# Optimization experiments

Measured on AMD Instinct MI355X. Metric: run time of the kernel, lower is better.

## Reference

```python
import jax, jax.numpy as jnp
import numpy as np
import math

B, S, IN_DIM, FEATURES = 4, 4096, 1024, 1024


def setup_inputs() -> dict:
    key = jax.random.key(0)
    kx, kk = jax.random.split(key)
    x = jax.random.normal(kx, (B, S, IN_DIM), dtype=jnp.float32)
    # bool kernel representing a +1/-1 binary weight matrix
    kernel = jax.random.randint(kk, (IN_DIM, FEATURES), 0, 2).astype(jnp.bool_)
    scale = jnp.float32(1.0 / math.sqrt(IN_DIM))  # nn.initializers.constant(1/sqrt(in_dim))
    return {"x": x, "kernel": kernel, "scale": scale}


def reference(x, kernel, scale):
    # conn_dense: bool kernel encodes +1 (True) / -1 (False) weights
    w = jnp.where(kernel, 1.0, -1.0).astype(x.dtype)  # [in_dim, features]
    # [b, s, in] @ [in, f] -> [b, s, f], then scalar scale
    return scale * jnp.einsum("bsi,if->bsf", x, w)
```

## Files before the change

### kernel.cpp

```cpp
#include <hip/hip_runtime.h>


#define M_TOT 16384
#define N_TOT 1024
#define K_TOT 1024

typedef __attribute__((ext_vector_type(8))) short bf16x8;
typedef __attribute__((ext_vector_type(4))) float f32x4;

__device__ __forceinline__ unsigned short f2bf(float f) {
    unsigned int u = __builtin_bit_cast(unsigned int, f);
    u += 0x7FFFu + ((u >> 16) & 1u);
    return (unsigned short)(u >> 16);
}

__global__ void detect_mode(const unsigned int* __restrict__ k32, int* __restrict__ flag) {
    __shared__ int s;
    if (threadIdx.x == 0) s = 0;
    __syncthreads();
    int bad = 0;
    for (int i = threadIdx.x; i < 1024; i += 256)
        if (k32[i] > 1u) bad = 1;
    if (bad) atomicOr(&s, 1);
    __syncthreads();
    if (threadIdx.x == 0) flag[0] = s;
}

__global__ __launch_bounds__(256) void convert_w(
    const void* __restrict__ w_raw, unsigned short* __restrict__ wt,
    const int* __restrict__ mode_p)
{
    __shared__ unsigned short tile[64 * 72];
    const int tid = threadIdx.x;
    const int k0 = (blockIdx.x & 15) * 64;
    const int n0 = (blockIdx.x >> 4) * 64;
    const int row = tid >> 2;
    const int seg = (tid & 3) * 16;

    if (mode_p[0] == 0) {
        const unsigned int* w = (const unsigned int*)w_raw;
        const uint4* src = reinterpret_cast<const uint4*>(
            w + (size_t)(k0 + row) * N_TOT + n0 + seg);
        #pragma unroll
        for (int q = 0; q < 4; ++q) {
            uint4 v = src[q];
            ushort4 h;
            h.x = v.x ? 0x3F80u : 0xBF80u;
            h.y = v.y ? 0x3F80u : 0xBF80u;
            h.z = v.z ? 0x3F80u : 0xBF80u;
            h.w = v.w ? 0x3F80u : 0xBF80u;
            *reinterpret_cast<ushort4*>(&tile[row * 72 + seg + q * 4]) = h;
        }
    } else {
        const unsigned char* w = (const unsigned char*)w_raw;
        uint4 v = *reinterpret_cast<const uint4*>(
            w + (size_t)(k0 + row) * N_TOT + n0 + seg);
        unsigned char b[16];
        *reinterpret_cast<uint4*>(b) = v;
        #pragma unroll
        for (int q = 0; q < 4; ++q) {
            ushort4 h;
            h.x = b[q * 4 + 0] ? 0x3F80u : 0xBF80u;
            h.y = b[q * 4 + 1] ? 0x3F80u : 0xBF80u;
            h.z = b[q * 4 + 2] ? 0x3F80u : 0xBF80u;
            h.w = b[q * 4 + 3] ? 0x3F80u : 0xBF80u;
            *reinterpret_cast<ushort4*>(&tile[row * 72 + seg + q * 4]) = h;
        }
    }
    __syncthreads();
    {
        int n = tid >> 2, kseg = (tid & 3) * 16;
        ushort4 o[4];
        #pragma unroll
        for (int j = 0; j < 16; ++j)
            ((unsigned short*)o)[j] = tile[(kseg + j) * 72 + n];
        ushort4* dst = reinterpret_cast<ushort4*>(wt + (size_t)(n0 + n) * K_TOT + k0 + kseg);
        dst[0] = o[0]; dst[1] = o[1]; dst[2] = o[2]; dst[3] = o[3];
    }
}

__global__ __launch_bounds__(256) void bf16_gemm(
    const float* __restrict__ X,
    const unsigned short* __restrict__ BT,
    const float* __restrict__ scale_p, float* __restrict__ out)
{
    __shared__ unsigned short As[128 * 64];
    __shared__ unsigned short Bs[128 * 64];

    const int tid  = threadIdx.x;
    const int lane = tid & 63;
    const int wave = tid >> 6;
    const int wm = (wave & 1) * 64;
    const int wn = (wave >> 1) * 64;

    const int j  = blockIdx.x & 7;
    const int s  = blockIdx.x >> 3;
    const int by = ((s >> 3) << 3) | j;
    const int bx = s & 7;
    const int m0 = by * 128, n0 = bx * 128;

    const int fr = lane & 15, fq = lane >> 4;
    const float scale = scale_p[0];

    const int srow = wave * 32 + (lane >> 3);
    const int skch = (lane & 7) ^ (lane >> 3);

    const int arow = tid >> 4;
    const int akseg = (tid & 15) * 4;
    const int achunk = (tid & 15) >> 1;
    const int ahalf = tid & 1;

    f32x4 acc[4][4] = {};

    for (int k0 = 0; k0 < K_TOT; k0 += 64) {
        #pragma unroll
        for (int q = 0; q < 4; ++q) {
            const unsigned short* g = BT + (size_t)(n0 + srow + q * 8) * K_TOT + k0 + skch * 8;
            __builtin_amdgcn_global_load_lds(
                (const __attribute__((address_space(1))) void*)g,
                (__attribute__((address_space(3))) void*)&Bs[wave * 2048 + q * 512],
                16, 0, 0);
        }
        #pragma unroll
        for (int q = 0; q < 8; ++q) {
            const int row = q * 16 + arow;
            const float4 v = *reinterpret_cast<const float4*>(
                X + (size_t)(m0 + row) * K_TOT + k0 + akseg);
            ushort4 h;
            h.x = f2bf(v.x); h.y = f2bf(v.y); h.z = f2bf(v.z); h.w = f2bf(v.w);
            const int slot = achunk ^ (row & 7);
            *reinterpret_cast<ushort4*>(&As[row * 64 + slot * 8 + ahalf * 4]) = h;
        }
        __syncthreads();

        #pragma unroll
        for (int ks = 0; ks < 2; ++ks) {
            bf16x8 af[4], bfr[4];
            #pragma unroll
            for (int mi = 0; mi < 4; ++mi) {
                int r  = wm + mi * 16 + fr;
                int ch = (ks * 4 + fq) ^ (r & 7);
                af[mi] = *reinterpret_cast<const bf16x8*>(&As[r * 64 + ch * 8]);
            }
            #pragma unroll
            for (int ni = 0; ni < 4; ++ni) {
                int r  = wn + ni * 16 + fr;
                int ch = (ks * 4 + fq) ^ (r & 7);
                bfr[ni] = *reinterpret_cast<const bf16x8*>(&Bs[r * 64 + ch * 8]);
            }
            #pragma unroll
            for (int mi = 0; mi < 4; ++mi)
                #pragma unroll
                for (int ni = 0; ni < 4; ++ni)
                    acc[mi][ni] = __builtin_amdgcn_mfma_f32_16x16x32_bf16(
                        af[mi], bfr[ni], acc[mi][ni], 0, 0, 0);
        }
        __syncthreads();
    }

    #pragma unroll
    for (int mi = 0; mi < 4; ++mi) {
        #pragma unroll
        for (int ni = 0; ni < 4; ++ni) {
            const int col  = n0 + wn + ni * 16 + fr;
            const int rowb = m0 + wm + mi * 16 + fq * 4;
            #pragma unroll
            for (int jj = 0; jj < 4; ++jj)
                out[(size_t)(rowb + jj) * N_TOT + col] = scale * acc[mi][ni][jj];
        }
    }
}

#define BKP 40
__global__ __launch_bounds__(256, 2) void binary_dense_gemm(
    const float* __restrict__ x, const int* __restrict__ kern,
    const float* __restrict__ scale_p, float* __restrict__ out)
{
    __shared__ unsigned short Asf[128 * BKP];
    __shared__ unsigned short Bsf[128 * BKP];
    const int tid = threadIdx.x, lane = tid & 63, wave = tid >> 6;
    const int wm = (wave & 1) * 64, wn = (wave >> 1) * 64;
    const int bx = blockIdx.x & 7, by = blockIdx.x >> 3;
    const int m0 = by * 128, n0 = bx * 128;
    const float scale = scale_p[0];
    const int fr = lane & 15, fq = lane >> 4;
    f32x4 acc[4][4] = {};
    for (int k0 = 0; k0 < K_TOT; k0 += 32) {
        #pragma unroll
        for (int i = 0; i < 4; ++i) {
            int slot = tid + i * 256, row = slot >> 3, kg = (slot & 7) << 2;
            const float4 v = *reinterpret_cast<const float4*>(x + (size_t)(m0 + row) * K_TOT + k0 + kg);
            ushort4 h;
            h.x = f2bf(v.x); h.y = f2bf(v.y); h.z = f2bf(v.z); h.w = f2bf(v.w);
            *reinterpret_cast<ushort4*>(&Asf[row * BKP + kg]) = h;
        }
        #pragma unroll
        for (int i = 0; i < 4; ++i) {
            int slot = tid + i * 256, nl = slot & 127, kg = (slot >> 7) << 2;
            ushort4 h;
            h.x = kern[(size_t)(k0 + kg + 0) * N_TOT + n0 + nl] ? 0x3F80u : 0xBF80u;
            h.y = kern[(size_t)(k0 + kg + 1) * N_TOT + n0 + nl] ? 0x3F80u : 0xBF80u;
            h.z = kern[(size_t)(k0 + kg + 2) * N_TOT + n0 + nl] ? 0x3F80u : 0xBF80u;
            h.w = kern[(size_t)(k0 + kg + 3) * N_TOT + n0 + nl] ? 0x3F80u : 0xBF80u;
            *reinterpret_cast<ushort4*>(&Bsf[nl * BKP + kg]) = h;
        }
        __syncthreads();
        bf16x8 af[4], bfr[4];
        #pragma unroll
        for (int mi = 0; mi < 4; ++mi)
            af[mi] = *reinterpret_cast<const bf16x8*>(&Asf[(wm + mi * 16 + fr) * BKP + fq * 8]);
        #pragma unroll
        for (int ni = 0; ni < 4; ++ni)
            bfr[ni] = *reinterpret_cast<const bf16x8*>(&Bsf[(wn + ni * 16 + fr) * BKP + fq * 8]);
        #pragma unroll
        for (int mi = 0; mi < 4; ++mi)
            #pragma unroll
            for (int ni = 0; ni < 4; ++ni)
                acc[mi][ni] = __builtin_amdgcn_mfma_f32_16x16x32_bf16(af[mi], bfr[ni], acc[mi][ni], 0, 0, 0);
        __syncthreads();
    }
    #pragma unroll
    for (int mi = 0; mi < 4; ++mi)
        #pragma unroll
        for (int ni = 0; ni < 4; ++ni) {
            const int col = n0 + wn + ni * 16 + fr;
            const int rowb = m0 + wm + mi * 16 + fq * 4;
            #pragma unroll
            for (int jj = 0; jj < 4; ++jj)
                out[(size_t)(rowb + jj) * N_TOT + col] = scale * acc[mi][ni][jj];
        }
}

extern "C" void kernel_launch(void* const* d_in, const int* in_sizes, int n_in,
                              void* d_out, int out_size, void* d_ws, size_t ws_size,
                              hipStream_t stream) {
    const float* x     = (const float*)d_in[0];
    const void*  kern  = d_in[1];
    const float* scale = (const float*)d_in[2];
    float*       out   = (float*)d_out;

    const size_t wt_bytes = (size_t)N_TOT * K_TOT * 2;
    const size_t flag_off = 256;
    if (ws_size >= flag_off + wt_bytes) {
        int*            flag = (int*)d_ws;
        unsigned short* wt   = (unsigned short*)((char*)d_ws + flag_off);
        hipLaunchKernelGGL(detect_mode, dim3(1), dim3(256), 0, stream,
                           (const unsigned int*)kern, flag);
        hipLaunchKernelGGL(convert_w, dim3(256), dim3(256), 0, stream, kern, wt, flag);
        hipLaunchKernelGGL(bf16_gemm, dim3(1024), dim3(256), 0, stream,
                           x, wt, scale, out);
    } else {
        hipLaunchKernelGGL(binary_dense_gemm, dim3(1024), dim3(256), 0, stream,
                           x, (const int*)kern, scale, out);
    }
}
```

Before: 176.3 us.

## Stage fp32 activations directly into LDS and convert to bf16 at fragment load

The A tile is no longer loaded into registers, converted to bf16 and stored to LDS. It is now copied as fp32 straight into LDS with global_load_lds, using an XOR swizzle over 16 chunks. Each wave converts to bf16 when it reads its MFMA fragments. This removes the register round-trip and the store instructions in the load phase, but doubles LDS use for A (32 KB) and repeats the conversion for every wave that reads the same rows, which may lower occupancy.

```diff
diff --git a/kernel.cpp b/kernel.cpp
--- a/kernel.cpp
+++ b/kernel.cpp
@@ -84,7 +84,7 @@
     const unsigned short* __restrict__ BT,
     const float* __restrict__ scale_p, float* __restrict__ out)
 {
-    __shared__ unsigned short As[128 * 64];
+    __shared__ float          Af[128 * 64];
     __shared__ unsigned short Bs[128 * 64];
 
     const int tid  = threadIdx.x;
@@ -102,20 +102,18 @@
     const int fr = lane & 15, fq = lane >> 4;
     const float scale = scale_p[0];
 
-    const int srow = wave * 32 + (lane >> 3);
-    const int skch = (lane & 7) ^ (lane >> 3);
-
-    const int arow = tid >> 4;
-    const int akseg = (tid & 15) * 4;
-    const int achunk = (tid & 15) >> 1;
-    const int ahalf = tid & 1;
+    const int brow = wave * 32 + (lane >> 3);
+    const int bkch = (lane & 7) ^ (lane >> 3);
+
+    const int arow_l = lane >> 4;
+    const int achnk_l = lane & 15;
 
     f32x4 acc[4][4] = {};
 
     for (int k0 = 0; k0 < K_TOT; k0 += 64) {
         #pragma unroll
         for (int q = 0; q < 4; ++q) {
-            const unsigned short* g = BT + (size_t)(n0 + srow + q * 8) * K_TOT + k0 + skch * 8;
+            const unsigned short* g = BT + (size_t)(n0 + brow + q * 8) * K_TOT + k0 + bkch * 8;
             __builtin_amdgcn_global_load_lds(
                 (const __attribute__((address_space(1))) void*)g,
                 (__attribute__((address_space(3))) void*)&Bs[wave * 2048 + q * 512],
@@ -123,13 +121,13 @@
         }
         #pragma unroll
         for (int q = 0; q < 8; ++q) {
-            const int row = q * 16 + arow;
-            const float4 v = *reinterpret_cast<const float4*>(
-                X + (size_t)(m0 + row) * K_TOT + k0 + akseg);
-            ushort4 h;
-            h.x = f2bf(v.x); h.y = f2bf(v.y); h.z = f2bf(v.z); h.w = f2bf(v.w);
-            const int slot = achunk ^ (row & 7);
-            *reinterpret_cast<ushort4*>(&As[row * 64 + slot * 8 + ahalf * 4]) = h;
+            const int r = wave * 32 + q * 4 + arow_l;
+            const int gch = achnk_l ^ (r & 15);
+            const float* g = X + (size_t)(m0 + r) * K_TOT + k0 + gch * 4;
+            __builtin_amdgcn_global_load_lds(
+                (const __attribute__((address_space(1))) void*)g,
+                (__attribute__((address_space(3))) void*)&Af[wave * 2048 + q * 256],
+                16, 0, 0);
         }
         __syncthreads();
 
@@ -138,14 +136,23 @@
             bf16x8 af[4], bfr[4];
             #pragma unroll
             for (int mi = 0; mi < 4; ++mi) {
-                int r  = wm + mi * 16 + fr;
-                int ch = (ks * 4 + fq) ^ (r & 7);
-                af[mi] = *reinterpret_cast<const bf16x8*>(&As[r * 64 + ch * 8]);
+                const int r = wm + mi * 16 + fr;
+                const int c = ks * 8 + fq * 2;
+                const f32x4 lo = *reinterpret_cast<const f32x4*>(
+                    &Af[r * 64 + ((c    ) ^ (r & 15)) * 4]);
+                const f32x4 hi = *reinterpret_cast<const f32x4*>(
+                    &Af[r * 64 + ((c + 1) ^ (r & 15)) * 4]);
+                bf16x8 h;
+                h[0] = (short)f2bf(lo[0]); h[1] = (short)f2bf(lo[1]);
+                h[2] = (short)f2bf(lo[2]); h[3] = (short)f2bf(lo[3]);
+                h[4] = (short)f2bf(hi[0]); h[5] = (short)f2bf(hi[1]);
+                h[6] = (short)f2bf(hi[2]); h[7] = (short)f2bf(hi[3]);
+                af[mi] = h;
             }
             #pragma unroll
             for (int ni = 0; ni < 4; ++ni) {
-                int r  = wn + ni * 16 + fr;
-                int ch = (ks * 4 + fq) ^ (r & 7);
+                const int r  = wn + ni * 16 + fr;
+                const int ch = (ks * 4 + fq) ^ (r & 7);
                 bfr[ni] = *reinterpret_cast<const bf16x8*>(&Bs[r * 64 + ch * 8]);
             }
             #pragma unroll
```

New measurement: 176.5 us. About the same (+0.1%).
